# Kernel optimization log

Hardware: AMD Instinct MI355X
Metric: run time of the kernel (lower is better)

Reference implementation:

```python
import jax, jax.numpy as jnp
import numpy as np

B, T_V, T_A = 128, 64, 128
E_V, E_A = 1024, 512
H, EMB, C = 1024, 512, 512  # C = input_size - embedding_size
IN = EMB + C               # RNN input size = 1024
VOCAB = 20000


def setup_inputs() -> dict:
    key = jax.random.key(0)
    ks = jax.random.split(key, 26)
    s = 0.02
    inp = {
        "input": jax.random.normal(ks[0], (B, 1, EMB), jnp.float32),
        "enc_visual": jax.random.normal(ks[1], (B, T_V, E_V), jnp.float32),
        "enc_audio": jax.random.normal(ks[2], (B, T_A, E_A), jnp.float32),
        "hidden_state": jax.random.normal(ks[3], (1, B, H), jnp.float32),
        "cell_state": jax.random.normal(ks[4], (1, B, H), jnp.float32),
        # visual attention (Bahdanau): W1:[C,H], W2:[C,E_V], W3:[1,C]
        "W_va1": s * jax.random.normal(ks[5], (C, H), jnp.float32),
        "W_va2": s * jax.random.normal(ks[6], (C, E_V), jnp.float32),
        "W_va3": s * jax.random.normal(ks[7], (1, C), jnp.float32),
        "W_venc": s * jax.random.normal(ks[8], (C, E_V), jnp.float32),
        # audio attention
        "W_aa1": s * jax.random.normal(ks[9], (C, H), jnp.float32),
        "W_aa2": s * jax.random.normal(ks[10], (C, E_A), jnp.float32),
        "W_aa3": s * jax.random.normal(ks[11], (1, C), jnp.float32),
        "W_aenc": s * jax.random.normal(ks[12], (C, E_A), jnp.float32),
        # cross-modal context attention (over 2 context vectors)
        "W_ca1": s * jax.random.normal(ks[13], (C, H), jnp.float32),
        "W_ca2": s * jax.random.normal(ks[14], (C, C), jnp.float32),
        "W_ca3": s * jax.random.normal(ks[15], (1, C), jnp.float32),
        # LSTM-style custom RNN cell params
        "W_ih": s * jax.random.normal(ks[16], (4 * H, IN), jnp.float32),
        "W_hh": s * jax.random.normal(ks[17], (4 * H, H), jnp.float32),
        "b_ih": jnp.zeros((4 * H,), jnp.float32),
        "b_hh": jnp.zeros((4 * H,), jnp.float32),
        # output projection
        "W_out": s * jax.random.normal(ks[18], (VOCAB, H), jnp.float32),
        "b_out": jnp.zeros((VOCAB,), jnp.float32),
    }
    return inp


def _attend(h, enc, W1, W2, W3):
    # h: [B,H]; enc: [B,T,E]. Vectorized Bahdanau attention (original loops over T).
    v1 = h @ W1.T                               # [B,C]
    v2 = jnp.einsum('bte,ce->btc', enc, W2)     # [B,T,C]
    scores = jnp.tanh(v1[:, None, :] + v2) @ W3.T  # [B,T,1]
    attn = jax.nn.softmax(scores[..., 0], axis=1)  # [B,T]
    return jnp.einsum('bt,bte->be', attn, enc)     # [B,E]


def reference(input, enc_visual, enc_audio, hidden_state, cell_state,
              W_va1, W_va2, W_va3, W_venc,
              W_aa1, W_aa2, W_aa3, W_aenc,
              W_ca1, W_ca2, W_ca3,
              W_ih, W_hh, b_ih, b_hh, W_out, b_out):
    h0 = hidden_state[0]   # [B,H]
    c0 = cell_state[0]     # [B,H]

    vc = _attend(h0, enc_visual, W_va1, W_va2, W_va3) @ W_venc.T  # [B,C]
    ac = _attend(h0, enc_audio, W_aa1, W_aa2, W_aa3) @ W_aenc.T   # [B,C]
    all_ctx = jnp.stack([vc, ac], axis=1)                         # [B,2,C]
    final_ctx = _attend(h0, all_ctx, W_ca1, W_ca2, W_ca3)         # [B,C]

    x = jnp.concatenate([input[:, 0, :], jnp.tanh(final_ctx)], axis=-1)  # [B,IN]
    gates = x @ W_ih.T + b_ih + h0 @ W_hh.T + b_hh                 # [B,4H]
    i, f, g, o = jnp.split(gates, 4, axis=-1)
    c_new = jax.nn.sigmoid(f) * c0 + jax.nn.sigmoid(i) * jnp.tanh(g)
    h_new = jax.nn.sigmoid(o) * jnp.tanh(c_new)

    logits = h_new @ W_out.T + b_out                               # [B,V]
    return (logits[:, None, :], h_new[None], c_new[None])
```

## Files before the change

kernel.cpp:

```cpp
#include <hip/hip_runtime.h>
#include <hip/hip_bf16.h>
#include <cstddef>

typedef __attribute__((ext_vector_type(8))) short short8;
typedef __attribute__((ext_vector_type(4))) float f32x4;

static __device__ __forceinline__ f32x4 ldg(const float* p) {
    return *(const f32x4*)p;
}

static __device__ __forceinline__ short8 pack8(f32x4 f0, f32x4 f1) {
    union { __hip_bfloat162 h[4]; short8 s; } u;
    u.h[0] = __float22bfloat162_rn(make_float2(f0.x, f0.y));
    u.h[1] = __float22bfloat162_rn(make_float2(f0.z, f0.w));
    u.h[2] = __float22bfloat162_rn(make_float2(f1.x, f1.y));
    u.h[3] = __float22bfloat162_rn(make_float2(f1.z, f1.w));
    return u.s;
}

static __device__ __forceinline__ void gload16(const short* g, short* l) {
    __builtin_amdgcn_global_load_lds(
        (const __attribute__((address_space(1))) void*)g,
        (__attribute__((address_space(3))) void*)l, 16, 0, 0);
}

static __device__ __forceinline__ float bflo(unsigned int u) {
    union { unsigned int i; float f; } c; c.i = u << 16; return c.f;
}
static __device__ __forceinline__ float bfhi(unsigned int u) {
    union { unsigned int i; float f; } c; c.i = u & 0xffff0000u; return c.f;
}

static __device__ __forceinline__ void lds_barrier() {
    asm volatile("s_waitcnt lgkmcnt(0)" ::: "memory");
    __builtin_amdgcn_s_barrier();
    asm volatile("" ::: "memory");
}

static __device__ __forceinline__ void sk_body(
    const float* __restrict__ A, int lda,
    const float* __restrict__ W,
    const float* __restrict__ bias, int addbias,
    float* __restrict__ C, int ldc, int N,
    int kbeg, int kend, int n0, int m0)
{
    __shared__ short As[2][128 * 32];
    __shared__ short Ws[2][64 * 32];
    const int tid  = threadIdx.x;
    const int lane = tid & 63;
    const int wave = tid >> 6;
    const int wm = wave * 32;

    f32x4 acc[2][4];
    #pragma unroll
    for (int i = 0; i < 2; ++i)
        #pragma unroll
        for (int j = 0; j < 4; ++j)
            acc[i][j] = (f32x4){0.f, 0.f, 0.f, 0.f};

    const int arow = tid >> 1;
    const int ah   = tid & 1;
    const int afs  = (arow >> 1) & 3;
    const float* gA = A + (size_t)(m0 + arow) * lda + kbeg + ah * 16;
    const int aoff0 = arow * 32 + (((ah * 2)     ^ afs) * 8);
    const int aoff1 = arow * 32 + (((ah * 2 + 1) ^ afs) * 8);

    const int wrow  = tid >> 2;
    const int wslot = tid & 3;
    const int wvalid = (n0 + wrow) < N;
    const float* gW = W + (size_t)n0 * lda + (size_t)wrow * lda + kbeg + wslot * 8;
    const int woff = wrow * 32 + ((wslot ^ ((wrow >> 1) & 3)) * 8);

    const int frow = lane & 15;
    const int hi   = lane >> 4;
    const int fsl  = (hi ^ ((frow >> 1) & 3)) * 8;
    const int ra   = (wm + frow) * 32 + fsl;
    const int rb   = frow * 32 + fsl;

    const int nsteps = (kend - kbeg) >> 5;

    f32x4 a0_[4], a1_[4], w0_[2], w1_[2];
    #pragma unroll
    for (int q = 0; q < 4; ++q) a0_[q] = ldg(gA + q * 4);
    #pragma unroll
    for (int q = 0; q < 4; ++q) a1_[q] = ldg(gA + 32 + q * 4);
    if (wvalid) {
        w0_[0] = ldg(gW);      w0_[1] = ldg(gW + 4);
        w1_[0] = ldg(gW + 32); w1_[1] = ldg(gW + 36);
    } else {
        w0_[0] = w0_[1] = w1_[0] = w1_[1] = (f32x4){0.f, 0.f, 0.f, 0.f};
    }

    for (int s = 0; s < nsteps; s += 2) {
        {
            short* as = As[0]; short* ws = Ws[0];
            *(short8*)(as + aoff0) = pack8(a0_[0], a0_[1]);
            *(short8*)(as + aoff1) = pack8(a0_[2], a0_[3]);
            *(short8*)(ws + woff)  = pack8(w0_[0], w0_[1]);
            if (s + 2 < nsteps) {
                const float* nA = gA + (s + 2) * 32;
                #pragma unroll
                for (int q = 0; q < 4; ++q) a0_[q] = ldg(nA + q * 4);
                if (wvalid) {
                    const float* nW = gW + (s + 2) * 32;
                    w0_[0] = ldg(nW); w0_[1] = ldg(nW + 4);
                }
            }
            lds_barrier();
            short8 af[2], bf[4];
            #pragma unroll
            for (int i = 0; i < 2; ++i) af[i] = *(const short8*)(as + ra + i * 512);
            #pragma unroll
            for (int j = 0; j < 4; ++j) bf[j] = *(const short8*)(ws + rb + j * 512);
            #pragma unroll
            for (int i = 0; i < 2; ++i)
                #pragma unroll
                for (int j = 0; j < 4; ++j)
                    acc[i][j] = __builtin_amdgcn_mfma_f32_16x16x32_bf16(af[i], bf[j], acc[i][j], 0, 0, 0);
        }
        {
            short* as = As[1]; short* ws = Ws[1];
            *(short8*)(as + aoff0) = pack8(a1_[0], a1_[1]);
            *(short8*)(as + aoff1) = pack8(a1_[2], a1_[3]);
            *(short8*)(ws + woff)  = pack8(w1_[0], w1_[1]);
            if (s + 3 < nsteps) {
                const float* nA = gA + (s + 3) * 32;
                #pragma unroll
                for (int q = 0; q < 4; ++q) a1_[q] = ldg(nA + q * 4);
                if (wvalid) {
                    const float* nW = gW + (s + 3) * 32;
                    w1_[0] = ldg(nW); w1_[1] = ldg(nW + 4);
                }
            }
            lds_barrier();
            short8 af[2], bf[4];
            #pragma unroll
            for (int i = 0; i < 2; ++i) af[i] = *(const short8*)(as + ra + i * 512);
            #pragma unroll
            for (int j = 0; j < 4; ++j) bf[j] = *(const short8*)(ws + rb + j * 512);
            #pragma unroll
            for (int i = 0; i < 2; ++i)
                #pragma unroll
                for (int j = 0; j < 4; ++j)
                    acc[i][j] = __builtin_amdgcn_mfma_f32_16x16x32_bf16(af[i], bf[j], acc[i][j], 0, 0, 0);
        }
    }

    const int cl = lane & 15;
    const int rq = hi * 4;
    #pragma unroll
    for (int j = 0; j < 4; ++j) {
        int gc = n0 + j * 16 + cl;
        if (gc >= N) continue;
        float b = addbias ? bias[gc] : 0.f;
        #pragma unroll
        for (int i = 0; i < 2; ++i) {
            int gr = m0 + wm + i * 16 + rq;
            #pragma unroll
            for (int r = 0; r < 4; ++r)
                atomicAdd(C + (size_t)(gr + r) * ldc + gc, acc[i][j][r] + b);
        }
    }
}

__global__ __launch_bounds__(256) void gemm_sk(
    const float* __restrict__ A, const float* __restrict__ W,
    const float* __restrict__ bias, float* __restrict__ C,
    int N, int K, int kchunk, int ldc)
{
    int kbeg = blockIdx.y * kchunk;
    sk_body(A, K, W, bias, bias != nullptr && blockIdx.y == 0,
            C, ldc, N, kbeg, kbeg + kchunk, blockIdx.x * 64, blockIdx.z * 128);
}

__global__ __launch_bounds__(256) void ctxproj_mfma(
    const float* __restrict__ attv, const float* __restrict__ Wv,
    const float* __restrict__ atta, const float* __restrict__ Wa,
    float* __restrict__ ctx)
{
    const float* A; const float* W; float* C; int lda, kb, ke;
    if (blockIdx.z == 0) { A = attv; W = Wv; C = ctx;       lda = 1024; kb = blockIdx.y * 128; ke = kb + 128; }
    else                 { A = atta; W = Wa; C = ctx + 512; lda = 512;  kb = blockIdx.y * 64;  ke = kb + 64;  }
    sk_body(A, lda, W, nullptr, 0, C, 1024, 512, kb, ke, blockIdx.x * 64, 0);
}

__global__ __launch_bounds__(256) void gates_mfma(
    const float* __restrict__ xb, const float* __restrict__ W_ih,
    const float* __restrict__ h0, const float* __restrict__ W_hh,
    float* __restrict__ gates)
{
    int pair = blockIdx.y >> 2;
    const float* A = pair ? h0 : xb;
    const float* W = pair ? W_hh : W_ih;
    int kb = (blockIdx.y & 3) * 256;
    sk_body(A, 1024, W, nullptr, 0, gates, 4096, 4096, kb, kb + 256, blockIdx.x * 64, 0);
}

__global__ __launch_bounds__(256) void cvt_hproj(
    const float* __restrict__ encv, const float* __restrict__ enca,
    const float* __restrict__ wv2,  const float* __restrict__ wa2,
    short* __restrict__ oev, short* __restrict__ oea,
    short* __restrict__ owv, short* __restrict__ owa,
    const float* __restrict__ h0,
    const float* __restrict__ Wva1, const float* __restrict__ Waa1,
    const float* __restrict__ Wca1, float* __restrict__ hbase)
{
    int bid = blockIdx.x;
    if (bid < 8576) {
        const float* src; short* dst; int lb;
        if (bid < 4096)      { src = encv; dst = oev; lb = bid; }
        else if (bid < 8192) { src = enca; dst = oea; lb = bid - 4096; }
        else if (bid < 8448) { src = wv2;  dst = owv; lb = bid - 8192; }
        else                 { src = wa2;  dst = owa; lb = bid - 8448; }
        size_t off = ((size_t)lb * 256 + threadIdx.x) * 8;
        f32x4 f0 = *(const f32x4*)(src + off);
        f32x4 f1 = *(const f32x4*)(src + off + 4);
        *(short8*)(dst + off) = pack8(f0, f1);
        return;
    }
    int lb = bid - 8576;
    int n0g = (lb % 24) * 64;
    int kid = lb / 24;
    int wsel = n0g >> 9;
    const float* W = (wsel == 0) ? Wva1 : (wsel == 1) ? Waa1 : Wca1;
    float* C = hbase + (size_t)wsel * 128 * 512;
    sk_body(h0, 1024, W, nullptr, 0, C, 512, 512, kid * 128, kid * 128 + 128, n0g & 511, 0);
}

__global__ __launch_bounds__(256) void scores_fused(
    const short* __restrict__ Av, const short* __restrict__ Wv,
    const float* __restrict__ hv1,  const float* __restrict__ W_va3,
    float* __restrict__ scv,
    const short* __restrict__ Aa, const short* __restrict__ Wa,
    const float* __restrict__ ha1,  const float* __restrict__ W_aa3,
    float* __restrict__ sca)
{
    __shared__ short As[3][4096];
    __shared__ short Ws[3][4096];

    const short *A, *W; const float *v1, *W3;
    float* sc;
    int K, tshift, n0, m0;
    int idx = blockIdx.x;
    if (idx < 256) {
        n0 = (idx >> 6) * 128;  m0 = (idx & 63) * 128;
        A = Av; W = Wv; v1 = hv1; W3 = W_va3; sc = scv;
        K = 1024; tshift = 6;
    } else {
        idx -= 256;
        n0 = (idx >> 7) * 128;  m0 = (idx & 127) * 128;
        A = Aa; W = Wa; v1 = ha1; W3 = W_aa3; sc = sca;
        K = 512; tshift = 7;
    }

    const int tid  = threadIdx.x;
    const int lane = tid & 63;
    const int wave = tid >> 6;
    const int wr = wave >> 1;
    const int wc = wave & 1;

    f32x4 acc[4][4];
    #pragma unroll
    for (int i = 0; i < 4; ++i)
        #pragma unroll
        for (int j = 0; j < 4; ++j)
            acc[i][j] = (f32x4){0.f, 0.f, 0.f, 0.f};

    const int srow = lane >> 2;
    const int slsw = (lane & 3) ^ ((lane >> 3) & 3);
    const short* gA0 = A + (size_t)(m0 + wave * 16 + srow) * K + slsw * 8;
    const short* gA1 = gA0 + (size_t)64 * K;
    const short* gW0 = W + (size_t)(n0 + wave * 16 + srow) * K + slsw * 8;
    const short* gW1 = gW0 + (size_t)64 * K;
    const int ldsw = wave * 512;

    const int frow = lane & 15;
    const int hi   = lane >> 4;
    const int fsl  = (hi ^ ((frow >> 1) & 3)) * 8;
    const int raBase = (wr * 64 + frow) * 32 + fsl;
    const int rbBase = (wc * 64 + frow) * 32 + fsl;

    const int nsteps = K >> 5;

    short* A0 = &As[0][0];
    short* W0 = &Ws[0][0];
    auto stage = [&](int buf, int koff) {
        gload16(gA0 + koff, A0 + buf * 4096 + ldsw);
        gload16(gA1 + koff, A0 + buf * 4096 + 2048 + ldsw);
        gload16(gW0 + koff, W0 + buf * 4096 + ldsw);
        gload16(gW1 + koff, W0 + buf * 4096 + 2048 + ldsw);
    };

    stage(0, 0);
    stage(1, 32);

    int b0 = 0, b1 = 1, b2 = 2;
    for (int s = 0; s < nsteps; ++s) {
        int kk = s + 2; if (kk > nsteps - 1) kk = nsteps - 1;
        stage(b2, kk * 32);
        asm volatile("s_waitcnt vmcnt(8)" ::: "memory");
        __builtin_amdgcn_s_barrier();
        __builtin_amdgcn_sched_barrier(0);

        const short* as = A0 + b0 * 4096;
        const short* ws = W0 + b0 * 4096;
        short8 af[4], bf[4];
        #pragma unroll
        for (int i = 0; i < 4; ++i) af[i] = *(const short8*)(as + raBase + i * 512);
        #pragma unroll
        for (int j = 0; j < 4; ++j) bf[j] = *(const short8*)(ws + rbBase + j * 512);
        #pragma unroll
        for (int i = 0; i < 4; ++i)
            #pragma unroll
            for (int j = 0; j < 4; ++j)
                acc[i][j] = __builtin_amdgcn_mfma_f32_16x16x32_bf16(af[i], bf[j], acc[i][j], 0, 0, 0);
        __builtin_amdgcn_sched_barrier(0);
        __builtin_amdgcn_s_barrier();
        int t = b0; b0 = b1; b1 = b2; b2 = t;
    }

    const int cl = lane & 15;
    const int rq = hi * 4;
    #pragma unroll
    for (int i = 0; i < 4; ++i) {
        #pragma unroll
        for (int r = 0; r < 4; ++r) {
            int gr = m0 + wr * 64 + i * 16 + rq + r;
            const float* v1row = v1 + (size_t)(gr >> tshift) * 512;
            float p = 0.f;
            #pragma unroll
            for (int j = 0; j < 4; ++j) {
                int gc = n0 + wc * 64 + j * 16 + cl;
                p += tanhf(v1row[gc] + acc[i][j][r]) * W3[gc];
            }
            p += __shfl_xor(p, 1, 64);
            p += __shfl_xor(p, 2, 64);
            p += __shfl_xor(p, 4, 64);
            p += __shfl_xor(p, 8, 64);
            if (cl == 0) atomicAdd(sc + gr, p);
        }
    }
}

__global__ __launch_bounds__(256) void attend_out2(
    const float* __restrict__ scv, const short* __restrict__ encv_bf, float* __restrict__ attv,
    const float* __restrict__ sca, const short* __restrict__ enca_bf, float* __restrict__ atta)
{
    const float* sc; const unsigned int* enc2; float* out;
    int T, E2, ec;
    if (blockIdx.y < 2) { sc = scv; enc2 = (const unsigned int*)encv_bf; out = attv;
                          T = 64;  E2 = 512; ec = blockIdx.y; }
    else                { sc = sca; enc2 = (const unsigned int*)enca_bf; out = atta;
                          T = 128; E2 = 256; ec = 0; }

    __shared__ float ew[128];
    __shared__ float raw[128];
    const int b = blockIdx.x, tid = threadIdx.x;
    if (tid < T) raw[tid] = sc[(size_t)b * T + tid];
    __syncthreads();
    float m = -1e30f;
    for (int t = 0; t < T; ++t) m = fmaxf(m, raw[t]);
    if (tid < T) ew[tid] = __expf(raw[tid] - m);
    __syncthreads();
    float sum = 0.f;
    for (int t = 0; t < T; ++t) sum += ew[t];
    const float inv = 1.f / sum;

    const int ep = ec * 256 + tid;
    const unsigned int* encb = enc2 + (size_t)b * T * E2 + ep;
    float a0 = 0.f, a1 = 0.f;
    for (int t = 0; t < T; ++t) {
        unsigned int u = encb[(size_t)t * E2];
        float w = ew[t];
        a0 += w * bflo(u);
        a1 += w * bfhi(u);
    }
    out[(size_t)b * E2 * 2 + ep * 2]     = a0 * inv;
    out[(size_t)b * E2 * 2 + ep * 2 + 1] = a1 * inv;
}

__global__ __launch_bounds__(256) void cross_kernel(
    const float* __restrict__ hc1, const float* __restrict__ v2c,
    const float* __restrict__ W3, const float* __restrict__ ctx,
    const float* __restrict__ inp, float* __restrict__ x)
{
    const int C = 512;
    __shared__ float red[256];
    __shared__ float aw[2];
    const int b = blockIdx.x, tid = threadIdx.x;

    float p0 = 0.f, p1 = 0.f;
    for (int c = tid; c < C; c += 256) {
        float h = hc1[(size_t)b * C + c], w = W3[c];
        p0 += tanhf(h + v2c[(size_t)(b * 2 + 0) * C + c]) * w;
        p1 += tanhf(h + v2c[(size_t)(b * 2 + 1) * C + c]) * w;
    }
    red[tid] = p0; __syncthreads();
    for (int s = 128; s; s >>= 1) { if (tid < s) red[tid] += red[tid + s]; __syncthreads(); }
    float s0 = red[0];
    __syncthreads();
    red[tid] = p1; __syncthreads();
    for (int s = 128; s; s >>= 1) { if (tid < s) red[tid] += red[tid + s]; __syncthreads(); }
    if (tid == 0) {
        float s1 = red[0];
        float m = fmaxf(s0, s1);
        float e0 = __expf(s0 - m), e1 = __expf(s1 - m);
        float inv = 1.f / (e0 + e1);
        aw[0] = e0 * inv; aw[1] = e1 * inv;
    }
    __syncthreads();
    float a0 = aw[0], a1 = aw[1];
    for (int c = tid; c < C; c += 256) {
        float fc = a0 * ctx[(size_t)(b * 2 + 0) * C + c]
                 + a1 * ctx[(size_t)(b * 2 + 1) * C + c];
        x[(size_t)b * 1024 + 512 + c] = tanhf(fc);
        x[(size_t)b * 1024 + c] = inp[(size_t)b * 512 + c];
    }
}

__global__ __launch_bounds__(256) void lstm_kernel(
    const float* __restrict__ gates, const float* __restrict__ c0,
    const float* __restrict__ b_ih, const float* __restrict__ b_hh,
    float* __restrict__ hout, float* __restrict__ cout)
{
    const int idx = blockIdx.x * 256 + threadIdx.x;
    const int b = idx >> 10, h = idx & 1023;
    const float* g = gates + (size_t)b * 4096;
    float gi = g[h]        + b_ih[h]        + b_hh[h];
    float gf = g[1024 + h] + b_ih[1024 + h] + b_hh[1024 + h];
    float gg = g[2048 + h] + b_ih[2048 + h] + b_hh[2048 + h];
    float go = g[3072 + h] + b_ih[3072 + h] + b_hh[3072 + h];
    float si = 1.f / (1.f + __expf(-gi));
    float sf = 1.f / (1.f + __expf(-gf));
    float so = 1.f / (1.f + __expf(-go));
    float cn = sf * c0[idx] + si * tanhf(gg);
    float hn = so * tanhf(cn);
    cout[idx] = cn;
    hout[idx] = hn;
}

extern "C" void kernel_launch(void* const* d_in, const int* in_sizes, int n_in,
                              void* d_out, int out_size, void* d_ws, size_t ws_size,
                              hipStream_t stream)
{
    const float* inp    = (const float*)d_in[0];
    const float* encv   = (const float*)d_in[1];
    const float* enca   = (const float*)d_in[2];
    const float* h0     = (const float*)d_in[3];
    const float* c0     = (const float*)d_in[4];
    const float* W_va1  = (const float*)d_in[5];
    const float* W_va2  = (const float*)d_in[6];
    const float* W_va3  = (const float*)d_in[7];
    const float* W_venc = (const float*)d_in[8];
    const float* W_aa1  = (const float*)d_in[9];
    const float* W_aa2  = (const float*)d_in[10];
    const float* W_aa3  = (const float*)d_in[11];
    const float* W_aenc = (const float*)d_in[12];
    const float* W_ca1  = (const float*)d_in[13];
    const float* W_ca2  = (const float*)d_in[14];
    const float* W_ca3  = (const float*)d_in[15];
    const float* W_ih   = (const float*)d_in[16];
    const float* W_hh   = (const float*)d_in[17];
    const float* b_ih   = (const float*)d_in[18];
    const float* b_hh   = (const float*)d_in[19];
    const float* W_out  = (const float*)d_in[20];
    const float* b_out  = (const float*)d_in[21];
    float* out = (float*)d_out;

    float* ws = (float*)d_ws;
    float* hv1  = ws;  ws += 128 * 512;
    float* ha1  = ws;  ws += 128 * 512;
    float* hc1  = ws;  ws += 128 * 512;
    float* scv  = ws;  ws += 128 * 64;
    float* sca  = ws;  ws += 128 * 128;
    float* ctx  = ws;  ws += 128 * 2 * 512;
    float* v2c  = ws;  ws += 128 * 2 * 512;
    float* gates= ws;  ws += (size_t)128 * 4096;
    size_t zero_floats = (size_t)(ws - (float*)d_ws);
    float* xb   = ws;  ws += 128 * 1024;
    float* attv = ws;  ws += 128 * 1024;
    float* atta = ws;  ws += 128 * 512;
    short* encv_bf = (short*)ws;  ws += 8388608 / 2;
    short* enca_bf = (short*)ws;  ws += 8388608 / 2;
    short* wv2_bf  = (short*)ws;  ws += 524288 / 2;
    short* wa2_bf  = (short*)ws;  ws += 262144 / 2;

    dim3 blk(256);

    hipMemsetAsync(d_ws, 0, zero_floats * sizeof(float), stream);
    hipMemsetAsync(out, 0, (size_t)128 * 20000 * sizeof(float), stream);

    cvt_hproj<<<dim3(8768), blk, 0, stream>>>(encv, enca, W_va2, W_aa2,
                                              encv_bf, enca_bf, wv2_bf, wa2_bf,
                                              h0, W_va1, W_aa1, W_ca1, hv1);
    scores_fused<<<dim3(768), blk, 0, stream>>>(encv_bf, wv2_bf, hv1, W_va3, scv,
                                                enca_bf, wa2_bf, ha1, W_aa3, sca);
    attend_out2<<<dim3(128, 3), blk, 0, stream>>>(scv, encv_bf, attv, sca, enca_bf, atta);
    ctxproj_mfma<<<dim3(8, 8, 2), blk, 0, stream>>>(attv, W_venc, atta, W_aenc, ctx);
    gemm_sk<<<dim3(8, 4, 2), blk, 0, stream>>>(ctx, W_ca2, nullptr, v2c, 512, 512, 128, 512);
    cross_kernel<<<128, blk, 0, stream>>>(hc1, v2c, W_ca3, ctx, inp, xb);
    gates_mfma<<<dim3(64, 8), blk, 0, stream>>>(xb, W_ih, h0, W_hh, gates);
    float* hout = out + 2560000;
    float* cout = out + 2560000 + 131072;
    lstm_kernel<<<512, blk, 0, stream>>>(gates, c0, b_ih, b_hh, hout, cout);
    gemm_sk<<<dim3(313, 2, 1), blk, 0, stream>>>(hout, W_out, b_out, out, 20000, 1024, 512, 20000);
}
```

Measured before the change: 377.4 us.

## Deepen weight register prefetch in GEMM body and double-buffer scores kernel

Result: no change. 381.1 us (+1.0%).

```diff
diff --git a/kernel.cpp b/kernel.cpp
--- a/kernel.cpp
+++ b/kernel.cpp
@@ -68,7 +68,7 @@
     const int wrow  = tid >> 2;
     const int wslot = tid & 3;
     const int wvalid = (n0 + wrow) < N;
-    const float* gW = W + (size_t)n0 * lda + (size_t)wrow * lda + kbeg + wslot * 8;
+    const float* gW = W + (size_t)(n0 + wrow) * lda + kbeg + wslot * 8;
     const int woff = wrow * 32 + ((wslot ^ ((wrow >> 1) & 3)) * 8);
 
     const int frow = lane & 15;
@@ -163,6 +163,115 @@
     }
 }
 
+#define SK4_STEP(P, ABUF, ASET, WSET)                                        \
+    {                                                                        \
+        short* as = As[ABUF]; short* ws = Ws[ABUF];                          \
+        *(short8*)(as + aoff0) = pack8(ASET[0], ASET[1]);                    \
+        *(short8*)(as + aoff1) = pack8(ASET[2], ASET[3]);                    \
+        *(short8*)(ws + woff)  = pack8(WSET[0], WSET[1]);                    \
+        if (s + P + 2 < nsteps) {                                            \
+            const float* nA = gA + (s + P + 2) * 32;                         \
+            ASET[0] = ldg(nA);     ASET[1] = ldg(nA + 4);                    \
+            ASET[2] = ldg(nA + 8); ASET[3] = ldg(nA + 12);                   \
+        }                                                                    \
+        if (wvalid && s + P + 4 < nsteps) {                                  \
+            const float* nW = gW + (s + P + 4) * 32;                         \
+            WSET[0] = ldg(nW); WSET[1] = ldg(nW + 4);                        \
+        }                                                                    \
+        lds_barrier();                                                       \
+        short8 af[2], bf[4];                                                 \
+        _Pragma("unroll")                                                    \
+        for (int i = 0; i < 2; ++i) af[i] = *(const short8*)(as + ra + i * 512); \
+        _Pragma("unroll")                                                    \
+        for (int j = 0; j < 4; ++j) bf[j] = *(const short8*)(ws + rb + j * 512); \
+        _Pragma("unroll")                                                    \
+        for (int i = 0; i < 2; ++i)                                          \
+            _Pragma("unroll")                                                \
+            for (int j = 0; j < 4; ++j)                                      \
+                acc[i][j] = __builtin_amdgcn_mfma_f32_16x16x32_bf16(af[i], bf[j], acc[i][j], 0, 0, 0); \
+    }
+
+static __device__ __forceinline__ void sk_body4(
+    const float* __restrict__ A, int lda,
+    const float* __restrict__ W,
+    const float* __restrict__ bias, int addbias,
+    float* __restrict__ C, int ldc, int N,
+    int kbeg, int kend, int n0, int m0)
+{
+    __shared__ short As[2][128 * 32];
+    __shared__ short Ws[2][64 * 32];
+    const int tid  = threadIdx.x;
+    const int lane = tid & 63;
+    const int wave = tid >> 6;
+    const int wm = wave * 32;
+
+    f32x4 acc[2][4];
+    #pragma unroll
+    for (int i = 0; i < 2; ++i)
+        #pragma unroll
+        for (int j = 0; j < 4; ++j)
+            acc[i][j] = (f32x4){0.f, 0.f, 0.f, 0.f};
+
+    const int arow = tid >> 1;
+    const int ah   = tid & 1;
+    const int afs  = (arow >> 1) & 3;
+    const float* gA = A + (size_t)(m0 + arow) * lda + kbeg + ah * 16;
+    const int aoff0 = arow * 32 + (((ah * 2)     ^ afs) * 8);
+    const int aoff1 = arow * 32 + (((ah * 2 + 1) ^ afs) * 8);
+
+    const int wrow  = tid >> 2;
+    const int wslot = tid & 3;
+    const int wvalid = (n0 + wrow) < N;
+    const float* gW = W + (size_t)(n0 + wrow) * lda + kbeg + wslot * 8;
+    const int woff = wrow * 32 + ((wslot ^ ((wrow >> 1) & 3)) * 8);
+
+    const int frow = lane & 15;
+    const int hi   = lane >> 4;
+    const int fsl  = (hi ^ ((frow >> 1) & 3)) * 8;
+    const int ra   = (wm + frow) * 32 + fsl;
+    const int rb   = frow * 32 + fsl;
+
+    const int nsteps = (kend - kbeg) >> 5;
+
+    f32x4 a0_[4], a1_[4], w0_[2], w1_[2], w2_[2], w3_[2];
+    #pragma unroll
+    for (int q = 0; q < 4; ++q) a0_[q] = ldg(gA + q * 4);
+    #pragma unroll
+    for (int q = 0; q < 4; ++q) a1_[q] = ldg(gA + 32 + q * 4);
+    if (wvalid) {
+        w0_[0] = ldg(gW);      w0_[1] = ldg(gW + 4);
+        w1_[0] = ldg(gW + 32); w1_[1] = ldg(gW + 36);
+        w2_[0] = ldg(gW + 64); w2_[1] = ldg(gW + 68);
+        w3_[0] = ldg(gW + 96); w3_[1] = ldg(gW + 100);
+    } else {
+        w0_[0] = w0_[1] = w1_[0] = w1_[1] = (f32x4){0.f, 0.f, 0.f, 0.f};
+        w2_[0] = w2_[1] = w3_[0] = w3_[1] = (f32x4){0.f, 0.f, 0.f, 0.f};
+    }
+
+    for (int s = 0; s < nsteps; s += 4) {
+        SK4_STEP(0, 0, a0_, w0_)
+        SK4_STEP(1, 1, a1_, w1_)
+        SK4_STEP(2, 0, a0_, w2_)
+        SK4_STEP(3, 1, a1_, w3_)
+    }
+
+    const int cl = lane & 15;
+    const int rq = hi * 4;
+    #pragma unroll
+    for (int j = 0; j < 4; ++j) {
+        int gc = n0 + j * 16 + cl;
+        if (gc >= N) continue;
+        float b = addbias ? bias[gc] : 0.f;
+        #pragma unroll
+        for (int i = 0; i < 2; ++i) {
+            int gr = m0 + wm + i * 16 + rq;
+            #pragma unroll
+            for (int r = 0; r < 4; ++r)
+                atomicAdd(C + (size_t)(gr + r) * ldc + gc, acc[i][j][r] + b);
+        }
+    }
+}
+
 __global__ __launch_bounds__(256) void gemm_sk(
     const float* __restrict__ A, const float* __restrict__ W,
     const float* __restrict__ bias, float* __restrict__ C,
@@ -173,6 +282,16 @@
             C, ldc, N, kbeg, kbeg + kchunk, blockIdx.x * 64, blockIdx.z * 128);
 }
 
+__global__ __launch_bounds__(256) void gemm_sk4(
+    const float* __restrict__ A, const float* __restrict__ W,
+    const float* __restrict__ bias, float* __restrict__ C,
+    int N, int K, int kchunk, int ldc)
+{
+    int kbeg = blockIdx.y * kchunk;
+    sk_body4(A, K, W, bias, bias != nullptr && blockIdx.y == 0,
+             C, ldc, N, kbeg, kbeg + kchunk, blockIdx.x * 64, blockIdx.z * 128);
+}
+
 __global__ __launch_bounds__(256) void ctxproj_mfma(
     const float* __restrict__ attv, const float* __restrict__ Wv,
     const float* __restrict__ atta, const float* __restrict__ Wa,
@@ -193,7 +312,7 @@
     const float* A = pair ? h0 : xb;
     const float* W = pair ? W_hh : W_ih;
     int kb = (blockIdx.y & 3) * 256;
-    sk_body(A, 1024, W, nullptr, 0, gates, 4096, 4096, kb, kb + 256, blockIdx.x * 64, 0);
+    sk_body4(A, 1024, W, nullptr, 0, gates, 4096, 4096, kb, kb + 256, blockIdx.x * 64, 0);
 }
 
 __global__ __launch_bounds__(256) void cvt_hproj(
@@ -235,8 +354,8 @@
     const float* __restrict__ ha1,  const float* __restrict__ W_aa3,
     float* __restrict__ sca)
 {
-    __shared__ short As[3][4096];
-    __shared__ short Ws[3][4096];
+    __shared__ short As[2][4096];
+    __shared__ short Ws[2][4096];
 
     const short *A, *W; const float *v1, *W3;
     float* sc;
@@ -282,28 +401,24 @@
 
     const int nsteps = K >> 5;
 
-    short* A0 = &As[0][0];
-    short* W0 = &Ws[0][0];
-    auto stage = [&](int buf, int koff) {
-        gload16(gA0 + koff, A0 + buf * 4096 + ldsw);
-        gload16(gA1 + koff, A0 + buf * 4096 + 2048 + ldsw);
-        gload16(gW0 + koff, W0 + buf * 4096 + ldsw);
-        gload16(gW1 + koff, W0 + buf * 4096 + 2048 + ldsw);
-    };
-
-    stage(0, 0);
-    stage(1, 32);
-
-    int b0 = 0, b1 = 1, b2 = 2;
+    gload16(gA0, As[0] + ldsw);
+    gload16(gA1, As[0] + 2048 + ldsw);
+    gload16(gW0, Ws[0] + ldsw);
+    gload16(gW1, Ws[0] + 2048 + ldsw);
+
+    int cur = 0;
     for (int s = 0; s < nsteps; ++s) {
-        int kk = s + 2; if (kk > nsteps - 1) kk = nsteps - 1;
-        stage(b2, kk * 32);
-        asm volatile("s_waitcnt vmcnt(8)" ::: "memory");
+        int nk = (s + 1 < nsteps ? s + 1 : s) * 32;
+        gload16(gA0 + nk, As[cur ^ 1] + ldsw);
+        gload16(gA1 + nk, As[cur ^ 1] + 2048 + ldsw);
+        gload16(gW0 + nk, Ws[cur ^ 1] + ldsw);
+        gload16(gW1 + nk, Ws[cur ^ 1] + 2048 + ldsw);
+        asm volatile("s_waitcnt vmcnt(4)" ::: "memory");
         __builtin_amdgcn_s_barrier();
         __builtin_amdgcn_sched_barrier(0);
 
-        const short* as = A0 + b0 * 4096;
-        const short* ws = W0 + b0 * 4096;
+        const short* as = As[cur];
+        const short* ws = Ws[cur];
         short8 af[4], bf[4];
         #pragma unroll
         for (int i = 0; i < 4; ++i) af[i] = *(const short8*)(as + raBase + i * 512);
@@ -316,7 +431,7 @@
                 acc[i][j] = __builtin_amdgcn_mfma_f32_16x16x32_bf16(af[i], bf[j], acc[i][j], 0, 0, 0);
         __builtin_amdgcn_sched_barrier(0);
         __builtin_amdgcn_s_barrier();
-        int t = b0; b0 = b1; b1 = b2; b2 = t;
+        cur ^= 1;
     }
 
     const int cl = lane & 15;
@@ -503,5 +618,5 @@
     float* hout = out + 2560000;
     float* cout = out + 2560000 + 131072;
     lstm_kernel<<<512, blk, 0, stream>>>(gates, c0, b_ih, b_hh, hout, cout);
-    gemm_sk<<<dim3(313, 2, 1), blk, 0, stream>>>(hout, W_out, b_out, out, 20000, 1024, 512, 20000);
-}
+    gemm_sk4<<<dim3(313, 2, 1), blk, 0, stream>>>(hout, W_out, b_out, out, 20000, 1024, 512, 20000);
+}
```
